# Performance work log

Measured on AMD Instinct MI355X. Metric: run time of the kernel, lower is better.

Reference implementation:

```python
import jax, jax.numpy as jnp
import numpy as np

SEQ = 784  # 28*28, hard-coded by the module's view() calls
RES_CH = 32
DILATIONS = [1, 2, 4, 8, 16] * 2  # layer_size=5, stack_size=2


def setup_inputs() -> dict:
    key = jax.random.key(0)
    ks = jax.random.split(key, 9)
    B = 2048
    s = 0.1
    return {
        "x": jax.random.normal(ks[0], (B, 1, 28, 28), dtype=jnp.float32),
        "w_causal": jax.random.normal(ks[1], (RES_CH, 1, 2), dtype=jnp.float32) * s,
        "b_causal": jax.random.normal(ks[2], (RES_CH,), dtype=jnp.float32) * s,
        "w_dil": jax.random.normal(ks[3], (10, 2 * RES_CH, RES_CH, 2), dtype=jnp.float32) * s,
        "b_dil": jax.random.normal(ks[4], (10, 2 * RES_CH), dtype=jnp.float32) * s,
        "w_res": jax.random.normal(ks[5], (10, RES_CH, RES_CH), dtype=jnp.float32) * s,
        "b_res": jax.random.normal(ks[6], (10, RES_CH), dtype=jnp.float32) * s,
        "w_out": jax.random.normal(ks[7], (1, RES_CH), dtype=jnp.float32) * s,
        "b_out": jax.random.normal(ks[8], (1,), dtype=jnp.float32) * s,
    }


def _shift_right(h, d):
    # causal left-pad by d, keep original length: out[:, :, t] = h[:, :, t - d]
    return jnp.pad(h, ((0, 0), (0, 0), (d, 0)))[:, :, :SEQ]


def reference(x, w_causal, b_causal, w_dil, b_dil, w_res, b_res, w_out, b_out):
    B = x.shape[0]
    h = x.reshape(B, 1, SEQ)
    # Mask-A causal conv (kernel=2, dilation=1, pad [2,0], drop last):
    # y[t] = W[:,:,0] @ x[t-2] + W[:,:,1] @ x[t-1]  (strictly causal)
    y = (
        jnp.einsum("oi,bit->bot", w_causal[:, :, 0], _shift_right(h, 2))
        + jnp.einsum("oi,bit->bot", w_causal[:, :, 1], _shift_right(h, 1))
        + b_causal[None, :, None]
    )
    h = y
    # Residual stack: Mask-B dilated conv -> gated tanh*sigmoid -> 1x1 conv -> residual add
    for i, d in enumerate(DILATIONS):
        z = (
            jnp.einsum("oi,bit->bot", w_dil[i, :, :, 0], _shift_right(h, d))
            + jnp.einsum("oi,bit->bot", w_dil[i, :, :, 1], h)
            + b_dil[i][None, :, None]
        )  # [B, 2*RES_CH, SEQ]
        o1, o2 = z[:, :RES_CH], z[:, RES_CH:]
        gated = jnp.tanh(o1) * jax.nn.sigmoid(o2)
        h = h + jnp.einsum("oi,bit->bot", w_res[i], gated) + b_res[i][None, :, None]
    logits = jnp.einsum("oi,bit->bot", w_out, h) + b_out[None, :, None]
    return logits.reshape(B, 1, 28, 28)
```

## Files before the change

kernel.cpp:

```cpp
#include <hip/hip_runtime.h>

#define SEQ   784
#define PADT  16
#define NROW  (PADT + 784)
#define NWAVE 8
#define BLK   (NWAVE * 64)
#define LDS_BYTES (NROW * 32 * 2)

#define WS_WR_OFF 81920
#define WS_BD_OFF 102400
#define SC_TANH (-2.885390082f)
#define SC_SIGM (-1.442695041f)

typedef __attribute__((ext_vector_type(8))) short  short8;
typedef __attribute__((ext_vector_type(4))) float  float4v;
typedef __attribute__((ext_vector_type(2))) float  float2v;
typedef __attribute__((ext_vector_type(2))) unsigned int uint2v;

#if __has_builtin(__builtin_amdgcn_cvt_pk_bf16_f32)
typedef __attribute__((ext_vector_type(2))) __bf16 bf16x2;
__device__ __forceinline__ unsigned int pk_rne(float lo, float hi) {
    union { bf16x2 v; unsigned int u; } r;
    r.v = __builtin_amdgcn_cvt_pk_bf16_f32(lo, hi);
    return r.u;
}
#else
__device__ __forceinline__ unsigned int pk_rne(float lo, float hi) {
    unsigned int a = __float_as_uint(lo);
    unsigned int b = __float_as_uint(hi);
    a += 0x7fffu + ((a >> 16) & 1u);
    b += 0x7fffu + ((b >> 16) & 1u);
    return __builtin_amdgcn_perm(b, a, 0x07060302);
}
#endif
__device__ __forceinline__ unsigned short f2bf(float f) {
    unsigned int a = __float_as_uint(f);
    a += 0x7fffu + ((a >> 16) & 1u);
    return (unsigned short)(a >> 16);
}
__device__ __forceinline__ void gate_pair(float a1, float b1, float a2, float b2,
                                          float& g1, float& g2) {
    float2v ta, tb;
    ta.x = __builtin_amdgcn_exp2f(a1); ta.y = __builtin_amdgcn_exp2f(a2);
    tb.x = __builtin_amdgcn_exp2f(b1); tb.y = __builtin_amdgcn_exp2f(b2);
    float2v p  = (1.0f + ta) * (1.0f + tb);
    float   r  = __builtin_amdgcn_rcpf(p.x * p.y);
    float2v ps; ps.x = p.y; ps.y = p.x;
    float2v g  = (1.0f - ta) * ps * r;
    g1 = g.x; g2 = g.y;
}

__global__ void __launch_bounds__(64) prep_kernel(
    const float* __restrict__ w_dil, const float* __restrict__ b_dil,
    const float* __restrict__ w_res, unsigned char* __restrict__ ws)
{
    const int L    = blockIdx.x;
    const int lane = threadIdx.x;
    const int m    = lane & 15;
    const int q    = lane >> 4;
    short8* WSA = (short8*)ws;
    short8* WSR = (short8*)(ws + WS_WR_OFF);
    float*  WSB = (float*)(ws + WS_BD_OFF);

    #pragma unroll
    for (int rt = 0; rt < 4; ++rt) {
        const float sc = (rt < 2) ? SC_TANH : SC_SIGM;
        const float4* wp = (const float4*)(w_dil + (((L * 64 + rt * 16 + m) * 32) + q * 8) * 2);
        float4 c0 = wp[0], c1 = wp[1], c2 = wp[2], c3 = wp[3];
        union { unsigned int i[4]; short8 v; } u0, u1;
        u0.i[0] = pk_rne(sc * c0.x, sc * c0.z); u0.i[1] = pk_rne(sc * c1.x, sc * c1.z);
        u0.i[2] = pk_rne(sc * c2.x, sc * c2.z); u0.i[3] = pk_rne(sc * c3.x, sc * c3.z);
        u1.i[0] = pk_rne(sc * c0.y, sc * c0.w); u1.i[1] = pk_rne(sc * c1.y, sc * c1.w);
        u1.i[2] = pk_rne(sc * c2.y, sc * c2.w); u1.i[3] = pk_rne(sc * c3.y, sc * c3.w);
        WSA[((L * 4 + rt) * 2 + 0) * 64 + lane] = u0.v;
        WSA[((L * 4 + rt) * 2 + 1) * 64 + lane] = u1.v;
    }
    #pragma unroll
    for (int rt = 0; rt < 2; ++rt) {
        const float4* wp = (const float4*)(w_res + (L * 32 + rt * 16 + m) * 32 + q * 8);
        float4 d0 = wp[0], d1 = wp[1];
        union { unsigned int i[4]; short8 v; } u;
        u.i[0] = pk_rne(d0.x, d0.y); u.i[1] = pk_rne(d0.z, d0.w);
        u.i[2] = pk_rne(d1.x, d1.y); u.i[3] = pk_rne(d1.z, d1.w);
        WSR[(L * 2 + rt) * 64 + lane] = u.v;
    }
    WSB[L * 64 + lane] = b_dil[L * 64 + lane] * ((lane < 32) ? SC_TANH : SC_SIGM);
}

__global__ void __launch_bounds__(BLK, 4) wavenet_kernel(
    const float* __restrict__ x,
    const float* __restrict__ w_causal,
    const float* __restrict__ b_causal,
    const float* __restrict__ b_res,
    const float* __restrict__ w_out,
    const float* __restrict__ b_out,
    const unsigned char* __restrict__ ws,
    float* __restrict__ out)
{
    extern __shared__ unsigned short lds[];
    unsigned short* H = lds;

    const int tid = threadIdx.x;
    const int b   = blockIdx.x;

    {
        unsigned int* p = (unsigned int*)H;
        if (tid < PADT * 16) p[tid] = 0u;
    }

    {
        int o = tid & 31;
        const int gsh = (o >> 3) << 3;
        const int oo  = o & 7;
        float wc0 = w_causal[o * 2 + 0];
        float wc1 = w_causal[o * 2 + 1];
        float bc  = b_causal[o];
        const float* xb = x + b * SEQ;
        for (int idx = tid; idx < SEQ * 32; idx += BLK) {
            int t = idx >> 5;
            float v = bc;
            if (t >= 2) v += wc0 * xb[t - 2];
            if (t >= 1) v += wc1 * xb[t - 1];
            int r = PADT + t;
            int sw = ((r >> 1) & 3) << 3;
            H[r * 32 + (gsh ^ sw) + oo] = f2bf(v);
        }
    }
    __syncthreads();

    const int lane = tid & 63;
    const int wave = tid >> 6;
    const int m    = lane & 15;
    const int q    = lane >> 4;
    const int adr1 = (32 * (q & 1) + m) * 4;
    const int adr2 = adr1 + 64;
    const int hi   = q >> 1;
    const int rowu0 = PADT + wave * 16 + m;
    const int su    = (rowu0 >> 1) & 3;
    const int offBu = ((q ^ su) << 3);
    const int offH1 = (((q >> 1) ^ su) << 3) + 4 * (q & 1);
    const int offH2 = ((((q >> 1) + 2) ^ su) << 3) + 4 * (q & 1);

    short8 I0, I1;
    #pragma unroll
    for (int j = 0; j < 8; ++j) {
        I0[j] = (q * 8 + j == m)      ? (short)0x3F80 : (short)0;
        I1[j] = (q * 8 + j == m + 16) ? (short)0x3F80 : (short)0;
    }

    const short8* WSA = (const short8*)ws;
    const short8* WSR = (const short8*)(ws + WS_WR_OFF);
    const float*  WSB = (const float*)(ws + WS_BD_OFF);

    const int dil[10] = {1, 2, 4, 8, 16, 1, 2, 4, 8, 16};

    for (int L = 0; L < 10; ++L) {
        const int d = dil[L];

        short8 WA[4][2], WR[2];
        #pragma unroll
        for (int rt = 0; rt < 4; ++rt) {
            WA[rt][0] = WSA[((L * 4 + rt) * 2 + 0) * 64 + lane];
            WA[rt][1] = WSA[((L * 4 + rt) * 2 + 1) * 64 + lane];
        }
        WR[0] = WSR[(L * 2 + 0) * 64 + lane];
        WR[1] = WSR[(L * 2 + 1) * 64 + lane];
        float4v BDv[4], BRv[2];
        #pragma unroll
        for (int rt = 0; rt < 4; ++rt)
            BDv[rt] = *(const float4v*)(WSB + L * 64 + rt * 16 + q * 4);
        #pragma unroll
        for (int rt = 0; rt < 2; ++rt) {
            const float* bp = b_res + L * 32 + rt * 16 + q * 4;
            BRv[rt] = (float4v){bp[0], bp[1], bp[2], bp[3]};
        }
        const int rs0   = rowu0 - d;
        const int offBs = ((q ^ ((rs0 >> 1) & 3)) << 3);

        auto do_tile = [&](int s, uint2v& n0, uint2v& n1) {
            const int rbase  = (rowu0 + s * (NWAVE * 16)) * 32;
            const int rbases = (rs0   + s * (NWAVE * 16)) * 32;
            const short8 Bs = *(const short8*)(H + rbases + offBs);
            const short8 Bu = *(const short8*)(H + rbase + offBu);

            float4v r0 = BRv[0], r1 = BRv[1];
            r0 = __builtin_amdgcn_mfma_f32_16x16x32_bf16(I0, Bu, r0, 0, 0, 0);
            r1 = __builtin_amdgcn_mfma_f32_16x16x32_bf16(I1, Bu, r1, 0, 0, 0);

            float4v a0 = BDv[0], a1 = BDv[1], a2 = BDv[2], a3 = BDv[3];
            a0 = __builtin_amdgcn_mfma_f32_16x16x32_bf16(WA[0][0], Bs, a0, 0, 0, 0);
            a0 = __builtin_amdgcn_mfma_f32_16x16x32_bf16(WA[0][1], Bu, a0, 0, 0, 0);
            a1 = __builtin_amdgcn_mfma_f32_16x16x32_bf16(WA[1][0], Bs, a1, 0, 0, 0);
            a1 = __builtin_amdgcn_mfma_f32_16x16x32_bf16(WA[1][1], Bu, a1, 0, 0, 0);
            a2 = __builtin_amdgcn_mfma_f32_16x16x32_bf16(WA[2][0], Bs, a2, 0, 0, 0);
            a2 = __builtin_amdgcn_mfma_f32_16x16x32_bf16(WA[2][1], Bu, a2, 0, 0, 0);
            a3 = __builtin_amdgcn_mfma_f32_16x16x32_bf16(WA[3][0], Bs, a3, 0, 0, 0);
            a3 = __builtin_amdgcn_mfma_f32_16x16x32_bf16(WA[3][1], Bu, a3, 0, 0, 0);

            float g00, g01, g02, g03, g10, g11, g12, g13;
            gate_pair(a0[0], a2[0], a0[1], a2[1], g00, g01);
            gate_pair(a0[2], a2[2], a0[3], a2[3], g02, g03);
            gate_pair(a1[0], a3[0], a1[1], a3[1], g10, g11);
            gate_pair(a1[2], a3[2], a1[3], a3[3], g12, g13);
            int P0 = (int)pk_rne(g00, g01), P1 = (int)pk_rne(g02, g03);
            int P2 = (int)pk_rne(g10, g11), P3 = (int)pk_rne(g12, g13);

            int A0 = __builtin_amdgcn_ds_bpermute(adr1, P0);
            int A1 = __builtin_amdgcn_ds_bpermute(adr1, P1);
            int A2 = __builtin_amdgcn_ds_bpermute(adr1, P2);
            int A3 = __builtin_amdgcn_ds_bpermute(adr1, P3);
            int C0 = __builtin_amdgcn_ds_bpermute(adr2, P0);
            int C1 = __builtin_amdgcn_ds_bpermute(adr2, P1);
            int C2 = __builtin_amdgcn_ds_bpermute(adr2, P2);
            int C3 = __builtin_amdgcn_ds_bpermute(adr2, P3);
            union { int i[4]; short8 v; } ug;
            ug.i[0] = hi ? A2 : A0; ug.i[1] = hi ? A3 : A1;
            ug.i[2] = hi ? C2 : C0; ug.i[3] = hi ? C3 : C1;
            const short8 Gf = ug.v;

            r0 = __builtin_amdgcn_mfma_f32_16x16x32_bf16(WR[0], Gf, r0, 0, 0, 0);
            r1 = __builtin_amdgcn_mfma_f32_16x16x32_bf16(WR[1], Gf, r1, 0, 0, 0);

            n0 = (uint2v){pk_rne(r0[0], r0[1]), pk_rne(r0[2], r0[3])};
            n1 = (uint2v){pk_rne(r1[0], r1[1]), pk_rne(r1[2], r1[3])};
        };
        auto store_tile = [&](int s, const uint2v& n0, const uint2v& n1) {
            const int rbase = (rowu0 + s * (NWAVE * 16)) * 32;
            *(uint2v*)(H + rbase + offH1) = n0;
            *(uint2v*)(H + rbase + offH2) = n1;
        };

        uint2v A0v[4], A1v[4], B0v[3], B1v[3];
        do_tile(3, A0v[0], A1v[0]);
        do_tile(4, A0v[1], A1v[1]);
        do_tile(5, A0v[2], A1v[2]);
        if (wave == 0) do_tile(6, A0v[3], A1v[3]);
        __syncthreads();
        store_tile(3, A0v[0], A1v[0]);
        store_tile(4, A0v[1], A1v[1]);
        store_tile(5, A0v[2], A1v[2]);
        if (wave == 0) store_tile(6, A0v[3], A1v[3]);
        do_tile(0, B0v[0], B1v[0]);
        do_tile(1, B0v[1], B1v[1]);
        do_tile(2, B0v[2], B1v[2]);
        __syncthreads();
        store_tile(0, B0v[0], B1v[0]);
        store_tile(1, B0v[1], B1v[1]);
        store_tile(2, B0v[2], B1v[2]);
        __syncthreads();
    }

    {
        float wo[32];
        #pragma unroll
        for (int k = 0; k < 32; ++k) wo[k] = w_out[k];
        float bo = b_out[0];
        for (int t = tid; t < SEQ; t += BLK) {
            int r = PADT + t;
            int sw = ((r >> 1) & 3) << 3;
            const unsigned short* hp = H + r * 32;
            float s = bo;
            #pragma unroll
            for (int kk = 0; kk < 32; kk += 4) {
                int c = ((((kk >> 3) << 3) ^ sw)) + (kk & 7);
                uint2v hh = *(const uint2v*)(hp + c);
                s += wo[kk]     * __uint_as_float(hh.x << 16);
                s += wo[kk + 1] * __uint_as_float(hh.x & 0xffff0000u);
                s += wo[kk + 2] * __uint_as_float(hh.y << 16);
                s += wo[kk + 3] * __uint_as_float(hh.y & 0xffff0000u);
            }
            out[b * SEQ + t] = s;
        }
    }
}

extern "C" void kernel_launch(void* const* d_in, const int* in_sizes, int n_in,
                              void* d_out, int out_size, void* d_ws, size_t ws_size,
                              hipStream_t stream) {
    const float* x        = (const float*)d_in[0];
    const float* w_causal = (const float*)d_in[1];
    const float* b_causal = (const float*)d_in[2];
    const float* w_dil    = (const float*)d_in[3];
    const float* b_dil    = (const float*)d_in[4];
    const float* w_res    = (const float*)d_in[5];
    const float* b_res    = (const float*)d_in[6];
    const float* w_out    = (const float*)d_in[7];
    const float* b_out    = (const float*)d_in[8];
    float* out = (float*)d_out;
    unsigned char* ws = (unsigned char*)d_ws;

    const int B = in_sizes[0] / SEQ;

    prep_kernel<<<10, 64, 0, stream>>>(w_dil, b_dil, w_res, ws);
    wavenet_kernel<<<B, BLK, LDS_BYTES, stream>>>(
        x, w_causal, b_causal, b_res, w_out, b_out, ws, out);
}
```

Measured before the change: 440.3 us.

## Assign contiguous tile ranges per wave and update in place in reverse order

Each wave now owns a contiguous range of 16-row tiles and walks it backwards. Because the causal shift only reaches back at most 16 rows, tiles can be overwritten in place without waiting for other waves. Only the first tile's shifted input, which lies in the previous wave's range, is read before a single barrier. This removes one block-wide barrier per layer and the register buffering of results between barriers, and it loads tiles in pairs to overlap LDS reads. The trade-off is that correctness now depends on the ordering argument that the dilation never exceeds the tile height.

```diff
diff --git a/kernel.cpp b/kernel.cpp
--- a/kernel.cpp
+++ b/kernel.cpp
@@ -135,11 +135,15 @@
     const int adr1 = (32 * (q & 1) + m) * 4;
     const int adr2 = adr1 + 64;
     const int hi   = q >> 1;
-    const int rowu0 = PADT + wave * 16 + m;
-    const int su    = (rowu0 >> 1) & 3;
+
+    const int su    = ((PADT + m) >> 1) & 3;
     const int offBu = ((q ^ su) << 3);
     const int offH1 = (((q >> 1) ^ su) << 3) + 4 * (q & 1);
     const int offH2 = ((((q >> 1) + 2) ^ su) << 3) + 4 * (q & 1);
+    const int rowu_base = (PADT + m) * 32;
+
+    const int t0 = (wave * 49) >> 3;
+    const int t1 = ((wave + 1) * 49) >> 3;
 
     short8 I0, I1;
     #pragma unroll
@@ -152,10 +156,9 @@
     const short8* WSR = (const short8*)(ws + WS_WR_OFF);
     const float*  WSB = (const float*)(ws + WS_BD_OFF);
 
-    const int dil[10] = {1, 2, 4, 8, 16, 1, 2, 4, 8, 16};
-
     for (int L = 0; L < 10; ++L) {
-        const int d = dil[L];
+        const int Lr = (L >= 5) ? (L - 5) : L;
+        const int d  = 1 << Lr;
 
         short8 WA[4][2], WR[2];
         #pragma unroll
@@ -174,15 +177,15 @@
             const float* bp = b_res + L * 32 + rt * 16 + q * 4;
             BRv[rt] = (float4v){bp[0], bp[1], bp[2], bp[3]};
         }
-        const int rs0   = rowu0 - d;
-        const int offBs = ((q ^ ((rs0 >> 1) & 3)) << 3);
-
-        auto do_tile = [&](int s, uint2v& n0, uint2v& n1) {
-            const int rbase  = (rowu0 + s * (NWAVE * 16)) * 32;
-            const int rbases = (rs0   + s * (NWAVE * 16)) * 32;
-            const short8 Bs = *(const short8*)(H + rbases + offBs);
-            const short8 Bu = *(const short8*)(H + rbase + offBu);
-
+
+        const int rs0       = PADT + m - d;
+        const int offBs     = ((q ^ ((rs0 >> 1) & 3)) << 3);
+        const int rows_base = rs0 * 32;
+
+        const short8 Bs0 = *(const short8*)(H + rows_base + t0 * 512 + offBs);
+        __syncthreads();
+
+        auto compute_store = [&](int T, const short8 Bs, const short8 Bu) {
             float4v r0 = BRv[0], r1 = BRv[1];
             r0 = __builtin_amdgcn_mfma_f32_16x16x32_bf16(I0, Bu, r0, 0, 0, 0);
             r1 = __builtin_amdgcn_mfma_f32_16x16x32_bf16(I1, Bu, r1, 0, 0, 0);
@@ -221,32 +224,29 @@
             r0 = __builtin_amdgcn_mfma_f32_16x16x32_bf16(WR[0], Gf, r0, 0, 0, 0);
             r1 = __builtin_amdgcn_mfma_f32_16x16x32_bf16(WR[1], Gf, r1, 0, 0, 0);
 
-            n0 = (uint2v){pk_rne(r0[0], r0[1]), pk_rne(r0[2], r0[3])};
-            n1 = (uint2v){pk_rne(r1[0], r1[1]), pk_rne(r1[2], r1[3])};
+            uint2v n0 = (uint2v){pk_rne(r0[0], r0[1]), pk_rne(r0[2], r0[3])};
+            uint2v n1 = (uint2v){pk_rne(r1[0], r1[1]), pk_rne(r1[2], r1[3])};
+            unsigned short* hp = H + rowu_base + T * 512;
+            *(uint2v*)(hp + offH1) = n0;
+            *(uint2v*)(hp + offH2) = n1;
         };
-        auto store_tile = [&](int s, const uint2v& n0, const uint2v& n1) {
-            const int rbase = (rowu0 + s * (NWAVE * 16)) * 32;
-            *(uint2v*)(H + rbase + offH1) = n0;
-            *(uint2v*)(H + rbase + offH2) = n1;
-        };
-
-        uint2v A0v[4], A1v[4], B0v[3], B1v[3];
-        do_tile(3, A0v[0], A1v[0]);
-        do_tile(4, A0v[1], A1v[1]);
-        do_tile(5, A0v[2], A1v[2]);
-        if (wave == 0) do_tile(6, A0v[3], A1v[3]);
-        __syncthreads();
-        store_tile(3, A0v[0], A1v[0]);
-        store_tile(4, A0v[1], A1v[1]);
-        store_tile(5, A0v[2], A1v[2]);
-        if (wave == 0) store_tile(6, A0v[3], A1v[3]);
-        do_tile(0, B0v[0], B1v[0]);
-        do_tile(1, B0v[1], B1v[1]);
-        do_tile(2, B0v[2], B1v[2]);
-        __syncthreads();
-        store_tile(0, B0v[0], B1v[0]);
-        store_tile(1, B0v[1], B1v[1]);
-        store_tile(2, B0v[2], B1v[2]);
+
+        int T = t1;
+        while (T - 2 >= t0) {
+            T -= 2;
+            const short8 BuH = *(const short8*)(H + rowu_base + (T + 1) * 512 + offBu);
+            const short8 BsH = *(const short8*)(H + rows_base + (T + 1) * 512 + offBs);
+            const short8 BuL = *(const short8*)(H + rowu_base + T * 512 + offBu);
+            short8 BsL;
+            if (T != t0) BsL = *(const short8*)(H + rows_base + T * 512 + offBs);
+            else         BsL = Bs0;
+            compute_store(T + 1, BsH, BuH);
+            compute_store(T,     BsL, BuL);
+        }
+        if (T > t0) {
+            const short8 BuL = *(const short8*)(H + rowu_base + t0 * 512 + offBu);
+            compute_store(t0, Bs0, BuL);
+        }
         __syncthreads();
     }
 
```

Result: slower. 465.6 us (+5.7%).
